# Kernel tuning notes

Measured on AMD Instinct MI355X. Metric: run time of the kernel, lower is better.

The kernel has to match this reference:

```python
import jax, jax.numpy as jnp
import numpy as np

NL, D, DI, N, R, K = 4, 256, 512, 16, 16, 4  # layers, d_model, d_inner, d_state, dt_rank, conv kernel


def setup_inputs() -> dict:
    key = jax.random.key(0)
    ks = jax.random.split(key, 10)
    b, nc, nt = 8, 256, 64
    xc = jax.random.normal(ks[0], (b, nc, D), jnp.float32)
    xt = jax.random.normal(ks[1], (b, nt, D), jnp.float32)
    ln_g = jnp.ones((NL, D), jnp.float32)
    ln_b = jnp.zeros((NL, D), jnp.float32)
    W_in = jax.random.normal(ks[2], (NL, D, 2 * DI), jnp.float32) * (D ** -0.5)
    W_conv = jax.random.normal(ks[3], (NL, DI, 1, K), jnp.float32) * 0.2
    b_conv = jnp.zeros((NL, DI), jnp.float32)
    W_x = jax.random.normal(ks[4], (NL, DI, R + 2 * N), jnp.float32) * (DI ** -0.5)
    W_dt = jax.random.normal(ks[5], (NL, R, DI), jnp.float32) * (R ** -0.5)
    b_dt = jax.random.normal(ks[6], (NL, DI), jnp.float32) * 0.5 - 4.0  # softplus ~ 0.02
    A_log = jnp.broadcast_to(jnp.log(jnp.arange(1, N + 1, dtype=jnp.float32)), (NL, DI, N)).copy()
    Dp = jnp.ones((NL, DI), jnp.float32)
    W_out = jax.random.normal(ks[7], (NL, DI, D), jnp.float32) * (DI ** -0.5)
    return dict(xc=xc, xt=xt, ln_g=ln_g, ln_b=ln_b, W_in=W_in, W_conv=W_conv, b_conv=b_conv,
                W_x=W_x, W_dt=W_dt, b_dt=b_dt, A_log=A_log, Dp=Dp, W_out=W_out)


def _mamba_layer(x, g, beta, Wi, Wc, bc, Wx, Wdt, bdt, Alog, Dvec, Wo):
    # x: [B, L, D]; pre-LN residual Mamba-1 block
    mu = jnp.mean(x, axis=-1, keepdims=True)
    var = jnp.var(x, axis=-1, keepdims=True)
    h = (x - mu) * jax.lax.rsqrt(var + 1e-5) * g + beta
    xz = h @ Wi                              # [B, L, 2*DI]
    xp, z = xz[..., :DI], xz[..., DI:]
    # causal depthwise conv1d
    xcv = jax.lax.conv_general_dilated(xp.transpose(0, 2, 1), Wc, (1,), [(K - 1, 0)],
                                       feature_group_count=DI,
                                       dimension_numbers=('NCH', 'OIH', 'NCH'))
    xcv = jax.nn.silu(xcv.transpose(0, 2, 1) + bc)  # [B, L, DI]
    dbl = xcv @ Wx                           # [B, L, R+2N]
    dt = jax.nn.softplus(dbl[..., :R] @ Wdt + bdt)   # [B, L, DI]
    Bm = dbl[..., R:R + N]                   # [B, L, N]
    Cm = dbl[..., R + N:]                    # [B, L, N]
    A = -jnp.exp(Alog)                       # [DI, N]

    def step(hst, inp):
        x_t, dt_t, b_t, c_t = inp            # [B,DI],[B,DI],[B,N],[B,N]
        dA = jnp.exp(dt_t[:, :, None] * A)   # [B, DI, N]
        hst = dA * hst + (dt_t * x_t)[:, :, None] * b_t[:, None, :]
        return hst, jnp.einsum('bdn,bn->bd', hst, c_t)

    h0 = jnp.zeros((x.shape[0], DI, N), x.dtype)
    _, ys = jax.lax.scan(step, h0, (xcv.transpose(1, 0, 2), dt.transpose(1, 0, 2),
                                    Bm.transpose(1, 0, 2), Cm.transpose(1, 0, 2)))
    y = ys.transpose(1, 0, 2) + xcv * Dvec
    y = y * jax.nn.silu(z)
    return x + y @ Wo


def reference(xc, xt, ln_g, ln_b, W_in, W_conv, b_conv, W_x, W_dt, b_dt, A_log, Dp, W_out):
    b, nc, d = xc.shape
    nt = xt.shape[1]
    # replicate context per target token: [b*nt, nc+1, d]
    xr = jnp.broadcast_to(xc[:, None], (b, nt, nc, d)).reshape(b * nt, nc, d)
    x = jnp.concatenate([xr, xt.reshape(b * nt, 1, d)], axis=1)
    for i in range(NL):
        x = _mamba_layer(x, ln_g[i], ln_b[i], W_in[i], W_conv[i], b_conv[i],
                         W_x[i], W_dt[i], b_dt[i], A_log[i], Dp[i], W_out[i])
    return x[:, -1, :].reshape(b, nt, d)
```

## Files before the change

kernel.cpp:

```cpp
#include <hip/hip_runtime.h>
#include <hip/hip_bf16.h>

#define D_     256
#define TWO_DI 1024
#define DI_    512
#define NSTATE 16
#define RR     16
#define NDBL   48
#define BSEQ   8
#define NC     256
#define NCHUNK 16
#define CLEN   16
#define CTX    2048
#define TGT    512

typedef __attribute__((ext_vector_type(8))) short short8v;
typedef __attribute__((ext_vector_type(8))) unsigned short ushort8v;
typedef __attribute__((ext_vector_type(4))) float floatx4;

__device__ __forceinline__ float siluf(float x) { return x / (1.f + __expf(-x)); }
__device__ __forceinline__ float softplusf(float x) {
  return fmaxf(x, 0.f) + log1pf(__expf(-fabsf(x)));
}
__device__ __forceinline__ unsigned short f2bf(float x) {
// ... 122 lines not shown
  const unsigned short* Bp = &Bt[(size_t)(n0 + srow) * K + schunk];
  ushort8v b0 = *reinterpret_cast<const ushort8v*>(Bp);
  ushort8v b1 = *reinterpret_cast<const ushort8v*>(Bp + 8);
  floatx4 acc[2][2] = {};
#pragma unroll
  for (int j = 0; j < 4; ++j) {
    __syncthreads();
    {
      ushort8v o0, o1;
#pragma unroll
      for (int i = 0; i < 4; ++i) {
        float4 v = xr[j][i];
        unsigned short e0 = f2bf(v.x), e1 = f2bf(v.y), e2 = f2bf(v.z), e3 = f2bf(v.w);
        if (i < 2) { o0[i*4] = (short)e0; o0[i*4+1] = (short)e1; o0[i*4+2] = (short)e2; o0[i*4+3] = (short)e3; }
        else { int jj = (i - 2) * 4; o1[jj] = (short)e0; o1[jj+1] = (short)e1; o1[jj+2] = (short)e2; o1[jj+3] = (short)e3; }
      }
      *reinterpret_cast<ushort8v*>(&As[srow][schunk])     = o0;
      *reinterpret_cast<ushort8v*>(&As[srow][schunk + 8]) = o1;
    }
    *reinterpret_cast<ushort8v*>(&Bs[srow][schunk])     = b0;
    *reinterpret_cast<ushort8v*>(&Bs[srow][schunk + 8]) = b1;
    __syncthreads();
    if (j < 3) {
      b0 = *reinterpret_cast<const ushort8v*>(Bp + j * 64 + 64);
      b1 = *reinterpret_cast<const ushort8v*>(Bp + j * 64 + 72);
    }
#pragma unroll
    for (int ks = 0; ks < 2; ++ks) {
      short8v af2[2], bf2v[2];
#pragma unroll
      for (int f = 0; f < 2; ++f)
        af2[f] = *reinterpret_cast<const short8v*>(&As[wr * 32 + f * 16 + lr][ks * 32 + kq * 8]);
#pragma unroll
      for (int g2 = 0; g2 < 2; ++g2)
        bf2v[g2] = *reinterpret_cast<const short8v*>(&Bs[wc * 32 + g2 * 16 + lr][ks * 32 + kq * 8]);
#pragma unroll
      for (int f = 0; f < 2; ++f)
#pragma unroll
        for (int g2 = 0; g2 < 2; ++g2)
          acc[f][g2] = __builtin_amdgcn_mfma_f32_16x16x32_bf16(af2[f], bf2v[g2], acc[f][g2], 0, 0, 0);
    }
  }
#pragma unroll
  for (int f = 0; f < 2; ++f)
#pragma unroll
    for (int g2 = 0; g2 < 2; ++g2) {
      int col = n0 + wc * 32 + g2 * 16 + lr;
      float c0v = cs0[col], bwv = bW[col];
#pragma unroll
      for (int r = 0; r < 4; ++r) {
        int rowl = wr * 32 + f * 16 + kq * 4 + r;
        int row  = m0 + rowl;
        float v = rstds[rowl] * (acc[f][g2][r] - mus[rowl] * c0v) + bwv;
        if (EPI == 0) {
          C[(size_t)row * N + col] = v;
        } else {
          int bb = row >> 6;
          if (col < DI_) {
            float sv = siluf(cconv[bb * DI_ + col] + v * Wc4[col * 4 + 3]);
            xcv_bf[(size_t)row * DI_ + col] = f2bf(sv);
          } else {
            zbuf[(size_t)row * DI_ + (col - DI_)] = v;
          }
        }
      }
    }
}

template<int EPI>
__global__ __launch_bounds__(256) void gemm_in_ln(
    const float* __restrict__ X, const unsigned short* __restrict__ Bt,
    const float* __restrict__ cs0, const float* __restrict__ bW,
    float* __restrict__ C,
    const float* __restrict__ cconv, const float* __restrict__ Wc4,
    unsigned short* __restrict__ xcv_bf, float* __restrict__ zbuf)
{
  __shared__ unsigned short As[64][72];
  __shared__ unsigned short Bs[64][72];
  __shared__ float mus[64], rstds[64];
  gemm_in_ln_body<EPI>(As, Bs, mus, rstds, blockIdx.x, blockIdx.y,
                       X, Bt, cs0, bW, C, cconv, Wc4, xcv_bf, zbuf);
}

__global__ __launch_bounds__(256) void fused_gemm_in_ln(
    const float* __restrict__ Xa, const unsigned short* __restrict__ Bta,
    const float* __restrict__ cs0a, const float* __restrict__ bWa,
    float* __restrict__ Ca,
    const float* __restrict__ Xb, const unsigned short* __restrict__ Btb,
    const float* __restrict__ cs0b, const float* __restrict__ bWb,
    const float* __restrict__ cconv, const float* __restrict__ Wc4,
    unsigned short* __restrict__ xcv_bf, float* __restrict__ zbuf)
{
  __shared__ unsigned short As[64][72];
  __shared__ unsigned short Bs[64][72];
  __shared__ float mus[64], rstds[64];
  int f = blockIdx.x;
  if (f < 512)
    gemm_in_ln_body<0>(As, Bs, mus, rstds, f & 15, f >> 4, Xa, Bta, cs0a, bWa,
                       Ca, nullptr, nullptr, nullptr, nullptr);
  else {
    f -= 512;
    gemm_in_ln_body<1>(As, Bs, mus, rstds, f & 15, f >> 4, Xb, Btb, cs0b, bWb,
                       nullptr, cconv, Wc4, xcv_bf, zbuf);
  }
}

__global__ __launch_bounds__(256) void gemm_out(
    const unsigned short* __restrict__ A, const unsigned short* __restrict__ Bt,
    const float* __restrict__ resid, float* __restrict__ C, int N, int K)
{
  __shared__ unsigned short As[64][72];
  __shared__ unsigned short Bs[64][72];
  int tid = threadIdx.x;
  int n0 = blockIdx.x * 64, m0 = blockIdx.y * 64;
  int w = tid >> 6, lane = tid & 63;
  int lr = lane & 15, kq = lane >> 4;
  int wr = w >> 1, wc = w & 1;
  int srow = tid >> 2, schunk = (tid & 3) * 16;
  const unsigned short* Ap = &A[(size_t)(m0 + srow) * K + schunk];
  const unsigned short* Bp = &Bt[(size_t)(n0 + srow) * K + schunk];
  ushort8v a0 = *reinterpret_cast<const ushort8v*>(Ap);
  ushort8v a1 = *reinterpret_cast<const ushort8v*>(Ap + 8);
  ushort8v b0 = *reinterpret_cast<const ushort8v*>(Bp);
  ushort8v b1 = *reinterpret_cast<const ushort8v*>(Bp + 8);
  floatx4 acc[2][2] = {};
  for (int k0 = 0; k0 < K; k0 += 64) {
    __syncthreads();
    *reinterpret_cast<ushort8v*>(&As[srow][schunk])     = a0;
    *reinterpret_cast<ushort8v*>(&As[srow][schunk + 8]) = a1;
    *reinterpret_cast<ushort8v*>(&Bs[srow][schunk])     = b0;
    *reinterpret_cast<ushort8v*>(&Bs[srow][schunk + 8]) = b1;
    __syncthreads();
    if (k0 + 64 < K) {
      a0 = *reinterpret_cast<const ushort8v*>(Ap + k0 + 64);
      a1 = *reinterpret_cast<const ushort8v*>(Ap + k0 + 72);
      b0 = *reinterpret_cast<const ushort8v*>(Bp + k0 + 64);
      b1 = *reinterpret_cast<const ushort8v*>(Bp + k0 + 72);
    }
#pragma unroll
    for (int ks = 0; ks < 2; ++ks) {
      short8v af[2], bf2v[2];
#pragma unroll
      for (int f = 0; f < 2; ++f)
        af[f] = *reinterpret_cast<const short8v*>(&As[wr * 32 + f * 16 + lr][ks * 32 + kq * 8]);
#pragma unroll
      for (int g2 = 0; g2 < 2; ++g2)
        bf2v[g2] = *reinterpret_cast<const short8v*>(&Bs[wc * 32 + g2 * 16 + lr][ks * 32 + kq * 8]);
#pragma unroll
      for (int f = 0; f < 2; ++f)
#pragma unroll
        for (int g2 = 0; g2 < 2; ++g2)
          acc[f][g2] = __builtin_amdgcn_mfma_f32_16x16x32_bf16(af[f], bf2v[g2], acc[f][g2], 0, 0, 0);
    }
  }
#pragma unroll
  for (int f = 0; f < 2; ++f)
#pragma unroll
    for (int g2 = 0; g2 < 2; ++g2) {
      int col = n0 + wc * 32 + g2 * 16 + lr;
#pragma unroll
      for (int r = 0; r < 4; ++r) {
        int row = m0 + wr * 32 + f * 16 + kq * 4 + r;
        float v = acc[f][g2][r] + resid[(size_t)row * N + col];
        C[(size_t)row * N + col] = v;
      }
    }
}

__device__ __forceinline__ void gemm_s_body(int bx, int by,
    const unsigned short* __restrict__ A, const unsigned short* __restrict__ Bt,
    const float* __restrict__ resid, float* __restrict__ C, int N, int K)
{
  __shared__ unsigned short As[32][72];
  __shared__ unsigned short Bs[32][72];
  int tid = threadIdx.x;
  int n0 = bx * 32, m0 = by * 32;
  int w = tid >> 6, lane = tid & 63;
  int lr = lane & 15, kq = lane >> 4;
  int wr = w >> 1, wc = w & 1;
  int srow = tid >> 3, schunk = (tid & 7) * 8;
  const unsigned short* Ap = &A[(size_t)(m0 + srow) * K + schunk];
  const unsigned short* Bp = &Bt[(size_t)(n0 + srow) * K + schunk];
  ushort8v a0 = *reinterpret_cast<const ushort8v*>(Ap);
  ushort8v b0 = *reinterpret_cast<const ushort8v*>(Bp);
  floatx4 acc = {};
  for (int k0 = 0; k0 < K; k0 += 64) {
    __syncthreads();
    *reinterpret_cast<ushort8v*>(&As[srow][schunk]) = a0;
    *reinterpret_cast<ushort8v*>(&Bs[srow][schunk]) = b0;
    __syncthreads();
    if (k0 + 64 < K) {
      a0 = *reinterpret_cast<const ushort8v*>(Ap + k0 + 64);
      b0 = *reinterpret_cast<const ushort8v*>(Bp + k0 + 64);
    }
#pragma unroll
    for (int ks = 0; ks < 2; ++ks) {
      short8v af = *reinterpret_cast<const short8v*>(&As[wr * 16 + lr][ks * 32 + kq * 8]);
      short8v bf = *reinterpret_cast<const short8v*>(&Bs[wc * 16 + lr][ks * 32 + kq * 8]);
      acc = __builtin_amdgcn_mfma_f32_16x16x32_bf16(af, bf, acc, 0, 0, 0);
    }
  }
  int col = n0 + wc * 16 + lr;
#pragma unroll
  for (int r = 0; r < 4; ++r) {
    int row = m0 + wr * 16 + kq * 4 + r;
    float v = acc[r] + resid[(size_t)row * N + col];
    C[(size_t)row * N + col] = v;
  }
}

__global__ __launch_bounds__(256) void gemm_s(
    const unsigned short* __restrict__ A, const unsigned short* __restrict__ Bt,
    const float* __restrict__ resid, float* __restrict__ C, int N, int K)
{
  gemm_s_body(blockIdx.x, blockIdx.y, A, Bt, resid, C, N, K);
}

__device__ __forceinline__ void conv_sp_body(int blk,
    const float* __restrict__ xz, const float* __restrict__ Wc,
    const float* __restrict__ bc, const unsigned short* __restrict__ Wxt,
    const float* __restrict__ WdtT, const float* __restrict__ bdt,
    const float* __restrict__ Aneg,
    unsigned short* __restrict__ xcvb, float* __restrict__ dtb,
    float* __restrict__ dblg, float* __restrict__ cconv,
    float* __restrict__ Sb, float* __restrict__ Pb)
{
  __shared__ unsigned short xcs[16][528];
  __shared__ float dbl_s[16][48];
  int seq = blk >> 4, ch = blk & 15;
  int tok0 = blk * 16;
  int tid = threadIdx.x;
  int base = ch * 16;
  float xv_t[2][16], dt_t[2][16];
#pragma unroll
  for (int hh = 0; hh < 2; ++hh) {
    int c = tid + hh * 256;
    const float4 wv = *reinterpret_cast<const float4*>(&Wc[c * 4]);
    float bcv = bc[c];
    const float* xzs = &xz[(size_t)(seq * NC) * TWO_DI + c];
    float r[19];
#pragma unroll
    for (int i = 0; i < 19; ++i) {
      int tl = base - 3 + i;
      r[i] = (tl >= 0) ? xzs[(size_t)tl * TWO_DI] : 0.f;
    }
#pragma unroll
    for (int t = 0; t < 16; ++t) {
      float a = bcv + r[t] * wv.x + r[t + 1] * wv.y + r[t + 2] * wv.z + r[t + 3] * wv.w;
      unsigned short sv = f2bf(siluf(a));
      xcs[t][c] = sv;
      xcvb[(size_t)(tok0 + t) * DI_ + c] = sv;
      xv_t[hh][t] = bf2f(sv);
    }
    if (ch == 15)
      cconv[seq * DI_ + c] = bcv + r[16] * wv.x + r[17] * wv.y + r[18] * wv.z;
  }
  __syncthreads();
  int w = tid >> 6, lane = tid & 63, lr = lane & 15, kq = lane >> 4;
  if (w < 3) {
    floatx4 acc = {};
#pragma unroll
    for (int kc = 0; kc < 16; ++kc) {
      short8v bb = *reinterpret_cast<const short8v*>(&Wxt[(size_t)(w * 16 + lr) * DI_ + kc * 32 + kq * 8]);
      short8v aa = *reinterpret_cast<const short8v*>(&xcs[lr][kc * 32 + kq * 8]);
      acc = __builtin_amdgcn_mfma_f32_16x16x32_bf16(aa, bb, acc, 0, 0, 0);
    }
#pragma unroll
    for (int r2 = 0; r2 < 4; ++r2) {
      int t = kq * 4 + r2, col = w * 16 + lr;
      dbl_s[t][col] = acc[r2];
      dblg[(size_t)(tok0 + t) * NDBL + col] = acc[r2];
    }
  }
  __syncthreads();
#pragma unroll
  for (int hh = 0; hh < 2; ++hh) {
    int c = tid + hh * 256;
    float wr_[16];
    const float4* wt4 = reinterpret_cast<const float4*>(&WdtT[c * 16]);
#pragma unroll
    for (int qq = 0; qq < 4; ++qq) {
      float4 v4 = wt4[qq];
      wr_[qq * 4] = v4.x; wr_[qq * 4 + 1] = v4.y; wr_[qq * 4 + 2] = v4.z; wr_[qq * 4 + 3] = v4.w;
    }
    float bv = bdt[c];
#pragma unroll
    for (int t = 0; t < 16; ++t) {
      float accd = bv;
#pragma unroll
      for (int r2 = 0; r2 < 16; ++r2) accd += dbl_s[t][r2] * wr_[r2];
      float dtv = softplusf(accd);
      dt_t[hh][t] = dtv;
      dtb[(size_t)(tok0 + t) * DI_ + c] = dtv;
    }
  }
#pragma unroll
  for (int hh = 0; hh < 2; ++hh) {
    int d = tid + hh * 256;
    float An[16];
    const float4* An4 = reinterpret_cast<const float4*>(&Aneg[d * NSTATE]);
#pragma unroll
    for (int qq = 0; qq < 4; ++qq) {
      float4 a = An4[qq];
      An[qq * 4] = a.x; An[qq * 4 + 1] = a.y; An[qq * 4 + 2] = a.z; An[qq * 4 + 3] = a.w;
    }
    float h_n[16], p_n[16];
#pragma unroll
    for (int n = 0; n < 16; ++n) { h_n[n] = 0.f; p_n[n] = 1.f; }
#pragma unroll
    for (int t = 0; t < 16; ++t) {
      float dtv  = dt_t[hh][t];
      float coef = dtv * xv_t[hh][t];
      float4 B0 = *reinterpret_cast<const float4*>(&dbl_s[t][RR]);
      float4 B1 = *reinterpret_cast<const float4*>(&dbl_s[t][RR + 4]);
      float4 B2 = *reinterpret_cast<const float4*>(&dbl_s[t][RR + 8]);
      float4 B3 = *reinterpret_cast<const float4*>(&dbl_s[t][RR + 12]);
      float Bv[16] = {B0.x, B0.y, B0.z, B0.w, B1.x, B1.y, B1.z, B1.w,
                      B2.x, B2.y, B2.z, B2.w, B3.x, B3.y, B3.z, B3.w};
#pragma unroll
      for (int n = 0; n < 16; ++n) {
        float dA = __expf(dtv * An[n]);
        h_n[n] = fmaf(dA, h_n[n], coef * Bv[n]);
        p_n[n] *= dA;
      }
    }
    size_t ob = ((size_t)blk * DI_ + d) * NSTATE;
#pragma unroll
    for (int qq = 0; qq < 4; ++qq) {
      *reinterpret_cast<float4*>(&Sb[ob + qq * 4]) =
          make_float4(h_n[qq*4], h_n[qq*4+1], h_n[qq*4+2], h_n[qq*4+3]);
      *reinterpret_cast<float4*>(&Pb[ob + qq * 4]) =
          make_float4(p_n[qq*4], p_n[qq*4+1], p_n[qq*4+2], p_n[qq*4+3]);
    }
  }
}

__global__ __launch_bounds__(256) void conv_sp_kern(
    const float* __restrict__ xz, const float* __restrict__ Wc,
    const float* __restrict__ bc, const unsigned short* __restrict__ Wxt,
    const float* __restrict__ WdtT, const float* __restrict__ bdt,
    const float* __restrict__ Aneg,
    unsigned short* __restrict__ xcvb, float* __restrict__ dtb,
    float* __restrict__ dblg, float* __restrict__ cconv,
    float* __restrict__ Sb, float* __restrict__ Pb)
{
  conv_sp_body(blockIdx.x, xz, Wc, bc, Wxt, WdtT, bdt, Aneg,
               xcvb, dtb, dblg, cconv, Sb, Pb);
}

__device__ __forceinline__ void sf_body(int b,
    const float* __restrict__ dblg, const unsigned short* __restrict__ xcvb,
    const float* __restrict__ xz, const float* __restrict__ dtb,
    const float* __restrict__ Sb, const float* __restrict__ Pb,
    const float* __restrict__ Aneg, const float* __restrict__ Dp,
    unsigned short* __restrict__ yb, float* __restrict__ hstate)
{
  int dg = b & 31, sc = b >> 5;
  int seq = sc >> 4, chunk = sc & 15;
  int tid = threadIdx.x;
  int tt = tid >> 4, cc = tid & 15;
  int tok0 = sc * CLEN;
  __shared__ float dts[16][17], xs[16][17], zs[16][17], Bsh[16][17], Csh[16][17], ys[16][17];
  dts[tt][cc] = dtb[(size_t)(tok0 + tt) * DI_ + dg * 16 + cc];
  xs[tt][cc]  = bf2f(xcvb[(size_t)(tok0 + tt) * DI_ + dg * 16 + cc]);
  zs[tt][cc]  = xz[(size_t)(tok0 + tt) * TWO_DI + DI_ + dg * 16 + cc];
  Bsh[tt][cc] = dblg[(size_t)(tok0 + tt) * NDBL + RR + cc];
  Csh[tt][cc] = dblg[(size_t)(tok0 + tt) * NDBL + RR + NSTATE + cc];
  __syncthreads();
  int dl = tt, n = cc;
  int d = dg * 16 + dl;
  float A  = Aneg[d * NSTATE + n];
  float Dv = Dp[d];
  float Bn[16], Cn[16];
#pragma unroll
  for (int t = 0; t < CLEN; ++t) { Bn[t] = Bsh[t][n]; Cn[t] = Csh[t][n]; }
  float h = 0.f;
  for (int c2 = 0; c2 < chunk; ++c2) {
    size_t o = ((size_t)(seq * NCHUNK + c2) * DI_ + d) * NSTATE + n;
    h = fmaf(Pb[o], h, Sb[o]);
  }
#pragma unroll
  for (int t = 0; t < CLEN; ++t) {
    float dtv = dts[t][dl];
    float xv  = xs[t][dl];
    float dA  = __expf(dtv * A);
    h = fmaf(dA, h, dtv * xv * Bn[t]);
    float p = h * Cn[t];
    p += __shfl_xor(p, 1); p += __shfl_xor(p, 2);
    p += __shfl_xor(p, 4); p += __shfl_xor(p, 8);
    if (n == 0) ys[t][dl] = (p + xv * Dv) * siluf(zs[t][dl]);
  }
  __syncthreads();
  yb[(size_t)(tok0 + tt) * DI_ + dg * 16 + cc] = f2bf(ys[tt][cc]);
  if (chunk == NCHUNK - 1)
    hstate[(size_t)seq * DI_ * NSTATE + d * NSTATE + n] = h;
}

__global__ __launch_bounds__(256) void scan_fin(
    const float* __restrict__ dblg, const unsigned short* __restrict__ xcvb,
    const float* __restrict__ xz, const float* __restrict__ dtb,
    const float* __restrict__ Sb, const float* __restrict__ Pb,
    const float* __restrict__ Aneg, const float* __restrict__ Dp,
    unsigned short* __restrict__ yb, float* __restrict__ hstate)
{
  sf_body(blockIdx.x, dblg, xcvb, xz, dtb, Sb, Pb, Aneg, Dp, yb, hstate);
}

__global__ __launch_bounds__(256) void fused_fin_gout(
    const unsigned short* __restrict__ Ag, const unsigned short* __restrict__ Btg,
    const float* __restrict__ residg, float* __restrict__ Cg,
    const float* __restrict__ dblg, const unsigned short* __restrict__ xcvb,
    const float* __restrict__ xz, const float* __restrict__ dtb,
    const float* __restrict__ Sb, const float* __restrict__ Pb,
    const float* __restrict__ Aneg, const float* __restrict__ Dp,
    unsigned short* __restrict__ yb, float* __restrict__ hstate)
{
  if (blockIdx.x < 128) {
    int f = blockIdx.x;
    gemm_s_body(f & 7, f >> 3, Ag, Btg, residg, Cg, D_, DI_);
  } else {
    sf_body(blockIdx.x - 128, dblg, xcvb, xz, dtb, Sb, Pb, Aneg, Dp, yb, hstate);
  }
}

__device__ __forceinline__ void ssm_body(int blk,
    const unsigned short* __restrict__ xcv_bf, const float* __restrict__ zbuf,
    const unsigned short* __restrict__ Wx, const float* __restrict__ WdtT_l,
    const float* __restrict__ bdt_l, const float* __restrict__ An_l,
    const float* __restrict__ Dp_l, const float* __restrict__ hs,
    unsigned short* __restrict__ ybf)
{
  __shared__ float dbl_s[16][48];
  int tg = blk >> 3, cg = blk & 7;
  int tok0 = tg * 16;
  int b = tg >> 2;
  int tid = threadIdx.x;
  int w = tid >> 6, lane = tid & 63, lr = lane & 15, kq = lane >> 4;
  if (w < 3) {
    floatx4 acc = {};
#pragma unroll
    for (int kc = 0; kc < 16; ++kc) {
      short8v bb = *reinterpret_cast<const short8v*>(&Wx[(size_t)(w * 16 + lr) * DI_ + kc * 32 + kq * 8]);
      short8v aa = *reinterpret_cast<const short8v*>(&xcv_bf[(size_t)(tok0 + lr) * DI_ + kc * 32 + kq * 8]);
      acc = __builtin_amdgcn_mfma_f32_16x16x32_bf16(aa, bb, acc, 0, 0, 0);
    }
#pragma unroll
    for (int r = 0; r < 4; ++r)
      dbl_s[kq * 4 + r][w * 16 + lr] = acc[r];
  }
  __syncthreads();
  int c = cg * 64 + (tid & 63);
  int t0 = (tid >> 6) * 4;
  float wdt_r[16], An[16], hr[16];
  const float4* wt4 = reinterpret_cast<const float4*>(&WdtT_l[c * 16]);
  const float4* An4 = reinterpret_cast<const float4*>(&An_l[c * NSTATE]);
  const float4* hr4 = reinterpret_cast<const float4*>(&hs[(size_t)b * DI_ * NSTATE + c * NSTATE]);
#pragma unroll
  for (int qq = 0; qq < 4; ++qq) {
    float4 wv = wt4[qq]; wdt_r[qq*4]=wv.x; wdt_r[qq*4+1]=wv.y; wdt_r[qq*4+2]=wv.z; wdt_r[qq*4+3]=wv.w;
    float4 a = An4[qq]; An[qq*4]=a.x; An[qq*4+1]=a.y; An[qq*4+2]=a.z; An[qq*4+3]=a.w;
    float4 hv = hr4[qq]; hr[qq*4]=hv.x; hr[qq*4+1]=hv.y; hr[qq*4+2]=hv.z; hr[qq*4+3]=hv.w;
  }
  float Dv = Dp_l[c], bv = bdt_l[c];
#pragma unroll
  for (int tt = 0; tt < 4; ++tt) {
    int t = t0 + tt;
    float accd = bv;
#pragma unroll
    for (int r = 0; r < 16; ++r) accd += dbl_s[t][r] * wdt_r[r];
    float dtv = softplusf(accd);
    float xv = bf2f(xcv_bf[(size_t)(tok0 + t) * DI_ + c]);
    float coef = dtv * xv;
    float y = 0.f;
#pragma unroll
    for (int n = 0; n < 16; ++n) {
      float hn = fmaf(__expf(dtv * An[n]), hr[n], coef * dbl_s[t][RR + n]);
      y = fmaf(hn, dbl_s[t][RR + NSTATE + n], y);
    }
    float yv = (y + xv * Dv) * siluf(zbuf[(size_t)(tok0 + t) * DI_ + c]);
    ybf[(size_t)(tok0 + t) * DI_ + c] = f2bf(yv);
  }
}

__global__ __launch_bounds__(256) void tgt_ssm2(
    const unsigned short* __restrict__ xcv_bf, const float* __restrict__ zbuf,
    const unsigned short* __restrict__ Wx, const float* __restrict__ WdtT_l,
    const float* __restrict__ bdt_l, const float* __restrict__ An_l,
    const float* __restrict__ Dp_l, const float* __restrict__ hs,
    unsigned short* __restrict__ ybf)
{
  ssm_body(blockIdx.x, xcv_bf, zbuf, Wx, WdtT_l, bdt_l, An_l, Dp_l, hs, ybf);
}

__global__ __launch_bounds__(256) void fused_convsp_ssm(
    const float* __restrict__ xz, const float* __restrict__ Wc,
    const float* __restrict__ bc, const unsigned short* __restrict__ WxtA,
    const float* __restrict__ WdtTA, const float* __restrict__ bdtA,
    const float* __restrict__ AnegA,
    unsigned short* __restrict__ xcvb, float* __restrict__ dtb,
    float* __restrict__ dblg, float* __restrict__ cconv,
    float* __restrict__ Sb, float* __restrict__ Pb,
    const unsigned short* __restrict__ xcv_bfB, const float* __restrict__ zbufB,
    const unsigned short* __restrict__ WxB, const float* __restrict__ WdtTB,
    const float* __restrict__ bdtB, const float* __restrict__ AnB,
    const float* __restrict__ DpB, const float* __restrict__ hsB,
    unsigned short* __restrict__ ybfB)
{
  if (blockIdx.x < BSEQ * NCHUNK)
    conv_sp_body(blockIdx.x, xz, Wc, bc, WxtA, WdtTA, bdtA, AnegA,
                 xcvb, dtb, dblg, cconv, Sb, Pb);
  else
    ssm_body(blockIdx.x - BSEQ * NCHUNK, xcv_bfB, zbufB, WxB, WdtTB, bdtB,
             AnB, DpB, hsB, ybfB);
}

extern "C" void kernel_launch(void* const* d_in, const int* in_sizes, int n_in,
                              void* d_out, int out_size, void* d_ws, size_t ws_size,
                              hipStream_t stream)
{
  const float* xc   = (const float*)d_in[0];
  const float* xt   = (const float*)d_in[1];
  const float* ln_g = (const float*)d_in[2];
  const float* ln_b = (const float*)d_in[3];
  const float* W_in = (const float*)d_in[4];
  const float* W_cv = (const float*)d_in[5];
  const float* b_cv = (const float*)d_in[6];
  const float* W_x  = (const float*)d_in[7];
  const float* W_dt = (const float*)d_in[8];
  const float* b_dt = (const float*)d_in[9];
  const float* Alog = (const float*)d_in[10];
  const float* Dp   = (const float*)d_in[11];
  const float* W_o  = (const float*)d_in[12];
  float* out = (float*)d_out;

  float* ws = (float*)d_ws;
  size_t off = 0;
  auto alloc = [&](size_t n) { float* p = ws + off; off += n; return p; };
  float* xz     = alloc((size_t)CTX * TWO_DI);
  float* dtb    = alloc((size_t)CTX * DI_);
  float* dblg   = alloc((size_t)CTX * NDBL);
  float* xcur   = alloc((size_t)CTX * D_);
  float* Sb     = alloc((size_t)BSEQ * NCHUNK * DI_ * NSTATE);
  float* Pb     = alloc((size_t)BSEQ * NCHUNK * DI_ * NSTATE);
  float* cconvT = alloc((size_t)4 * BSEQ * DI_);
  float* hst    = alloc((size_t)4 * BSEQ * DI_ * NSTATE);
  float* Aneg   = alloc((size_t)4 * DI_ * NSTATE);
  float* WdtT   = alloc((size_t)4 * DI_ * RR);
  float* cs0b   = alloc((size_t)4 * TWO_DI);
  float* bWb    = alloc((size_t)4 * TWO_DI);
  float* zbufB  = alloc((size_t)TGT * DI_);
  float* xtb    = alloc((size_t)TGT * D_);
  unsigned short* xcvb    = (unsigned short*)alloc((size_t)CTX * DI_ / 2);
  unsigned short* yb_bf   = (unsigned short*)alloc((size_t)CTX * DI_ / 2);
  unsigned short* xcv_bfB = (unsigned short*)alloc((size_t)TGT * DI_ / 2);
  unsigned short* y_bfB   = (unsigned short*)alloc((size_t)TGT * DI_ / 2);
  unsigned short* Wint    = (unsigned short*)alloc((size_t)4 * TWO_DI * D_ / 2);
  unsigned short* Wot     = (unsigned short*)alloc((size_t)4 * D_ * DI_ / 2);
  unsigned short* Wxt     = (unsigned short*)alloc((size_t)4 * NDBL * DI_ / 2);
  if (off * sizeof(float) > ws_size) return;

  hipMemsetAsync(cs0b, 0, (size_t)8 * TWO_DI * sizeof(float), stream);
  prep_all<<<1920, 256, 0, stream>>>(W_in, W_o, W_x, Alog, W_dt, ln_g, ln_b,
                                     Wint, Wot, Wxt, Aneg, WdtT, cs0b, bWb);

  gemm_in_ln<0><<<dim3(16, CTX / 64), 256, 0, stream>>>(
      xc, Wint, cs0b, bWb, xz, nullptr, nullptr, nullptr, nullptr);
  conv_sp_kern<<<BSEQ * NCHUNK, 256, 0, stream>>>(
      xz, W_cv, b_cv, Wxt, WdtT, b_dt, Aneg, xcvb, dtb, dblg, cconvT, Sb, Pb);
  scan_fin<<<BSEQ * NCHUNK * 32, 256, 0, stream>>>(
      dblg, xcvb, xz, dtb, Sb, Pb, Aneg, Dp, yb_bf, hst);
  gemm_out<<<dim3(D_ / 64, CTX / 64), 256, 0, stream>>>(
      yb_bf, Wot, xc, xcur, D_, DI_);

  for (int l = 0; l < 3; ++l) {
    int la = l + 1;
    const float* xinB = (l == 0) ? xt : xtb;
    fused_gemm_in_ln<<<512 + 128, 256, 0, stream>>>(
        xcur, Wint + (size_t)la * TWO_DI * D_, cs0b + la * TWO_DI, bWb + la * TWO_DI, xz,
        xinB, Wint + (size_t)l * TWO_DI * D_, cs0b + l * TWO_DI, bWb + l * TWO_DI,
        cconvT + (size_t)l * BSEQ * DI_, W_cv + l * DI_ * 4, xcv_bfB, zbufB);
    fused_convsp_ssm<<<BSEQ * NCHUNK + 256, 256, 0, stream>>>(
        xz, W_cv + la * DI_ * 4, b_cv + la * DI_, Wxt + (size_t)la * NDBL * DI_,
        WdtT + (size_t)la * DI_ * RR, b_dt + la * DI_, Aneg + la * DI_ * NSTATE,
        xcvb, dtb, dblg, cconvT + (size_t)la * BSEQ * DI_, Sb, Pb,
        xcv_bfB, zbufB, Wxt + (size_t)l * NDBL * DI_, WdtT + (size_t)l * DI_ * RR,
        b_dt + l * DI_, Aneg + l * DI_ * NSTATE, Dp + l * DI_,
        hst + (size_t)l * BSEQ * DI_ * NSTATE, y_bfB);
    fused_fin_gout<<<128 + BSEQ * NCHUNK * 32, 256, 0, stream>>>(
        y_bfB, Wot + (size_t)l * D_ * DI_, xinB, xtb,
        dblg, xcvb, xz, dtb, Sb, Pb, Aneg + la * DI_ * NSTATE, Dp + la * DI_,
        yb_bf, hst + (size_t)la * BSEQ * DI_ * NSTATE);
    if (la < 3)
      gemm_out<<<dim3(D_ / 64, CTX / 64), 256, 0, stream>>>(
          yb_bf, Wot + (size_t)la * D_ * DI_, xcur, xcur, D_, DI_);
  }

  gemm_in_ln<1><<<dim3(16, TGT / 64), 256, 0, stream>>>(
      xtb, Wint + (size_t)3 * TWO_DI * D_, cs0b + 3 * TWO_DI, bWb + 3 * TWO_DI, nullptr,
      cconvT + (size_t)3 * BSEQ * DI_, W_cv + 3 * DI_ * 4, xcv_bfB, zbufB);
  tgt_ssm2<<<256, 256, 0, stream>>>(xcv_bfB, zbufB,
      Wxt + (size_t)3 * NDBL * DI_, WdtT + (size_t)3 * DI_ * RR, b_dt + 3 * DI_,
      Aneg + 3 * DI_ * NSTATE, Dp + 3 * DI_,
      hst + (size_t)3 * BSEQ * DI_ * NSTATE, y_bfB);
  gemm_s<<<dim3(D_ / 32, TGT / 32), 256, 0, stream>>>(
      y_bfB, Wot + (size_t)3 * D_ * DI_, xtb, out, D_, DI_);
}
```

Measured before the change: 337.0 us.

## Split chunk-local state scan out of conv kernel into a widely parallel kernel

Moves the per-chunk partial scan (chunk-end state S and decay product P) out of the conv kernel. There it ran serially per channel over 16 states in only 128 blocks. It now runs in a separate kernel with 4096 blocks, one thread per (channel, state), which reads dt, xcv and B back from global memory. The intent is to spread the exp-heavy scan across more of the GPU instead of a few register-heavy blocks. In exchange it adds a kernel launch per layer, plus global round-trips of dt, xcv and B, and the scan_fin work is no longer fused with the output GEMM.

```diff
diff --git a/kernel.cpp b/kernel.cpp
--- a/kernel.cpp
+++ b/kernel.cpp
@@ -362,14 +362,12 @@
   gemm_s_body(blockIdx.x, blockIdx.y, A, Bt, resid, C, N, K);
 }
 
-__device__ __forceinline__ void conv_sp_body(int blk,
+__device__ __forceinline__ void conv_body_lean(int blk,
     const float* __restrict__ xz, const float* __restrict__ Wc,
     const float* __restrict__ bc, const unsigned short* __restrict__ Wxt,
     const float* __restrict__ WdtT, const float* __restrict__ bdt,
-    const float* __restrict__ Aneg,
     unsigned short* __restrict__ xcvb, float* __restrict__ dtb,
-    float* __restrict__ dblg, float* __restrict__ cconv,
-    float* __restrict__ Sb, float* __restrict__ Pb)
+    float* __restrict__ dblg, float* __restrict__ cconv)
 {
   __shared__ unsigned short xcs[16][528];
   __shared__ float dbl_s[16][48];
@@ -377,7 +375,6 @@
   int tok0 = blk * 16;
   int tid = threadIdx.x;
   int base = ch * 16;
-  float xv_t[2][16], dt_t[2][16];
 #pragma unroll
   for (int hh = 0; hh < 2; ++hh) {
     int c = tid + hh * 256;
@@ -392,11 +389,10 @@
     }
 #pragma unroll
     for (int t = 0; t < 16; ++t) {
-      float a = bcv + r[t] * wv.x + r[t + 1] * wv.y + r[t + 2] * wv.z + r[t + 3] * wv.w;
-      unsigned short sv = f2bf(siluf(a));
+      float acc = bcv + r[t] * wv.x + r[t + 1] * wv.y + r[t + 2] * wv.z + r[t + 3] * wv.w;
+      unsigned short sv = f2bf(siluf(acc));
       xcs[t][c] = sv;
       xcvb[(size_t)(tok0 + t) * DI_ + c] = sv;
-      xv_t[hh][t] = bf2f(sv);
     }
     if (ch == 15)
       cconv[seq * DI_ + c] = bcv + r[16] * wv.x + r[17] * wv.y + r[18] * wv.z;
@@ -425,9 +421,9 @@
     float wr_[16];
     const float4* wt4 = reinterpret_cast<const float4*>(&WdtT[c * 16]);
 #pragma unroll
-    for (int qq = 0; qq < 4; ++qq) {
-      float4 v4 = wt4[qq];
-      wr_[qq * 4] = v4.x; wr_[qq * 4 + 1] = v4.y; wr_[qq * 4 + 2] = v4.z; wr_[qq * 4 + 3] = v4.w;
+    for (int q = 0; q < 4; ++q) {
+      float4 v4 = wt4[q];
+      wr_[q * 4] = v4.x; wr_[q * 4 + 1] = v4.y; wr_[q * 4 + 2] = v4.z; wr_[q * 4 + 3] = v4.w;
     }
     float bv = bdt[c];
 #pragma unroll
@@ -435,72 +431,84 @@
       float accd = bv;
 #pragma unroll
       for (int r2 = 0; r2 < 16; ++r2) accd += dbl_s[t][r2] * wr_[r2];
-      float dtv = softplusf(accd);
-      dt_t[hh][t] = dtv;
-      dtb[(size_t)(tok0 + t) * DI_ + c] = dtv;
-    }
-  }
-#pragma unroll
-  for (int hh = 0; hh < 2; ++hh) {
-    int d = tid + hh * 256;
-    float An[16];
-    const float4* An4 = reinterpret_cast<const float4*>(&Aneg[d * NSTATE]);
-#pragma unroll
-    for (int qq = 0; qq < 4; ++qq) {
-      float4 a = An4[qq];
-      An[qq * 4] = a.x; An[qq * 4 + 1] = a.y; An[qq * 4 + 2] = a.z; An[qq * 4 + 3] = a.w;
-    }
-    float h_n[16], p_n[16];
-#pragma unroll
-    for (int n = 0; n < 16; ++n) { h_n[n] = 0.f; p_n[n] = 1.f; }
-#pragma unroll
-    for (int t = 0; t < 16; ++t) {
-      float dtv  = dt_t[hh][t];
-      float coef = dtv * xv_t[hh][t];
-      float4 B0 = *reinterpret_cast<const float4*>(&dbl_s[t][RR]);
-      float4 B1 = *reinterpret_cast<const float4*>(&dbl_s[t][RR + 4]);
-      float4 B2 = *reinterpret_cast<const float4*>(&dbl_s[t][RR + 8]);
-      float4 B3 = *reinterpret_cast<const float4*>(&dbl_s[t][RR + 12]);
-      float Bv[16] = {B0.x, B0.y, B0.z, B0.w, B1.x, B1.y, B1.z, B1.w,
-                      B2.x, B2.y, B2.z, B2.w, B3.x, B3.y, B3.z, B3.w};
-#pragma unroll
-      for (int n = 0; n < 16; ++n) {
-        float dA = __expf(dtv * An[n]);
-        h_n[n] = fmaf(dA, h_n[n], coef * Bv[n]);
-        p_n[n] *= dA;
-      }
-    }
-    size_t ob = ((size_t)blk * DI_ + d) * NSTATE;
-#pragma unroll
-    for (int qq = 0; qq < 4; ++qq) {
-      *reinterpret_cast<float4*>(&Sb[ob + qq * 4]) =
-          make_float4(h_n[qq*4], h_n[qq*4+1], h_n[qq*4+2], h_n[qq*4+3]);
-      *reinterpret_cast<float4*>(&Pb[ob + qq * 4]) =
-          make_float4(p_n[qq*4], p_n[qq*4+1], p_n[qq*4+2], p_n[qq*4+3]);
-    }
-  }
-}
-
-__global__ __launch_bounds__(256) void conv_sp_kern(
+      dtb[(size_t)(tok0 + t) * DI_ + c] = softplusf(accd);
+    }
+  }
+}
+
+__global__ __launch_bounds__(256) void conv_lean_kern(
     const float* __restrict__ xz, const float* __restrict__ Wc,
     const float* __restrict__ bc, const unsigned short* __restrict__ Wxt,
     const float* __restrict__ WdtT, const float* __restrict__ bdt,
-    const float* __restrict__ Aneg,
     unsigned short* __restrict__ xcvb, float* __restrict__ dtb,
-    float* __restrict__ dblg, float* __restrict__ cconv,
+    float* __restrict__ dblg, float* __restrict__ cconv)
+{
+  conv_body_lean(blockIdx.x, xz, Wc, bc, Wxt, WdtT, bdt, xcvb, dtb, dblg, cconv);
+}
+
+__device__ __forceinline__ void sp_body(int b,
+    const float* __restrict__ dblg, const unsigned short* __restrict__ xcvb,
+    const float* __restrict__ dtb, const float* __restrict__ Aneg,
     float* __restrict__ Sb, float* __restrict__ Pb)
 {
-  conv_sp_body(blockIdx.x, xz, Wc, bc, Wxt, WdtT, bdt, Aneg,
-               xcvb, dtb, dblg, cconv, Sb, Pb);
-}
-
-__device__ __forceinline__ void sf_body(int b,
+  int dg = b & 31, sc = b >> 5;
+  int tid = threadIdx.x;
+  int tt = tid >> 4, cc = tid & 15;
+  int tok0 = sc * CLEN;
+  __shared__ float dts[16][17], xs[16][17], Bsh[16][17];
+  dts[tt][cc] = dtb[(size_t)(tok0 + tt) * DI_ + dg * 16 + cc];
+  xs[tt][cc]  = bf2f(xcvb[(size_t)(tok0 + tt) * DI_ + dg * 16 + cc]);
+  Bsh[tt][cc] = dblg[(size_t)(tok0 + tt) * NDBL + RR + cc];
+  __syncthreads();
+  int dl = tt, n = cc;
+  int d = dg * 16 + dl;
+  float A = Aneg[d * NSTATE + n];
+  float Bn[16];
+#pragma unroll
+  for (int t = 0; t < CLEN; ++t) Bn[t] = Bsh[t][n];
+  float h = 0.f, p = 1.f;
+#pragma unroll
+  for (int t = 0; t < CLEN; ++t) {
+    float dtv = dts[t][dl];
+    float dA  = __expf(dtv * A);
+    h = fmaf(dA, h, dtv * xs[t][dl] * Bn[t]);
+    p *= dA;
+  }
+  size_t o = ((size_t)sc * DI_ + d) * NSTATE + n;
+  Sb[o] = h; Pb[o] = p;
+}
+
+__global__ __launch_bounds__(256) void sp_kern(
+    const float* __restrict__ dblg, const unsigned short* __restrict__ xcvb,
+    const float* __restrict__ dtb, const float* __restrict__ Aneg,
+    float* __restrict__ Sb, float* __restrict__ Pb)
+{
+  sp_body(blockIdx.x, dblg, xcvb, dtb, Aneg, Sb, Pb);
+}
+
+__global__ __launch_bounds__(256) void fused_sp_gout(
+    const unsigned short* __restrict__ Ag, const unsigned short* __restrict__ Btg,
+    const float* __restrict__ residg, float* __restrict__ Cg,
+    const float* __restrict__ dblg, const unsigned short* __restrict__ xcvb,
+    const float* __restrict__ dtb, const float* __restrict__ Aneg,
+    float* __restrict__ Sb, float* __restrict__ Pb)
+{
+  if (blockIdx.x < 128) {
+    int f = blockIdx.x;
+    gemm_s_body(f & 7, f >> 3, Ag, Btg, residg, Cg, D_, DI_);
+  } else {
+    sp_body(blockIdx.x - 128, dblg, xcvb, dtb, Aneg, Sb, Pb);
+  }
+}
+
+__global__ __launch_bounds__(256) void scan_fin(
     const float* __restrict__ dblg, const unsigned short* __restrict__ xcvb,
     const float* __restrict__ xz, const float* __restrict__ dtb,
     const float* __restrict__ Sb, const float* __restrict__ Pb,
     const float* __restrict__ Aneg, const float* __restrict__ Dp,
     unsigned short* __restrict__ yb, float* __restrict__ hstate)
 {
+  int b = blockIdx.x;
   int dg = b & 31, sc = b >> 5;
   int seq = sc >> 4, chunk = sc & 15;
   int tid = threadIdx.x;
@@ -542,33 +550,6 @@
     hstate[(size_t)seq * DI_ * NSTATE + d * NSTATE + n] = h;
 }
 
-__global__ __launch_bounds__(256) void scan_fin(
-    const float* __restrict__ dblg, const unsigned short* __restrict__ xcvb,
-    const float* __restrict__ xz, const float* __restrict__ dtb,
-    const float* __restrict__ Sb, const float* __restrict__ Pb,
-    const float* __restrict__ Aneg, const float* __restrict__ Dp,
-    unsigned short* __restrict__ yb, float* __restrict__ hstate)
-{
-  sf_body(blockIdx.x, dblg, xcvb, xz, dtb, Sb, Pb, Aneg, Dp, yb, hstate);
-}
-
-__global__ __launch_bounds__(256) void fused_fin_gout(
-    const unsigned short* __restrict__ Ag, const unsigned short* __restrict__ Btg,
-    const float* __restrict__ residg, float* __restrict__ Cg,
-    const float* __restrict__ dblg, const unsigned short* __restrict__ xcvb,
-    const float* __restrict__ xz, const float* __restrict__ dtb,
-    const float* __restrict__ Sb, const float* __restrict__ Pb,
-    const float* __restrict__ Aneg, const float* __restrict__ Dp,
-    unsigned short* __restrict__ yb, float* __restrict__ hstate)
-{
-  if (blockIdx.x < 128) {
-    int f = blockIdx.x;
-    gemm_s_body(f & 7, f >> 3, Ag, Btg, residg, Cg, D_, DI_);
-  } else {
-    sf_body(blockIdx.x - 128, dblg, xcvb, xz, dtb, Sb, Pb, Aneg, Dp, yb, hstate);
-  }
-}
-
 __device__ __forceinline__ void ssm_body(int blk,
     const unsigned short* __restrict__ xcv_bf, const float* __restrict__ zbuf,
     const unsigned short* __restrict__ Wx, const float* __restrict__ WdtT_l,
@@ -638,14 +619,12 @@
   ssm_body(blockIdx.x, xcv_bf, zbuf, Wx, WdtT_l, bdt_l, An_l, Dp_l, hs, ybf);
 }
 
-__global__ __launch_bounds__(256) void fused_convsp_ssm(
+__global__ __launch_bounds__(256) void fused_conv_ssm(
     const float* __restrict__ xz, const float* __restrict__ Wc,
     const float* __restrict__ bc, const unsigned short* __restrict__ WxtA,
     const float* __restrict__ WdtTA, const float* __restrict__ bdtA,
-    const float* __restrict__ AnegA,
     unsigned short* __restrict__ xcvb, float* __restrict__ dtb,
     float* __restrict__ dblg, float* __restrict__ cconv,
-    float* __restrict__ Sb, float* __restrict__ Pb,
     const unsigned short* __restrict__ xcv_bfB, const float* __restrict__ zbufB,
     const unsigned short* __restrict__ WxB, const float* __restrict__ WdtTB,
     const float* __restrict__ bdtB, const float* __restrict__ AnB,
@@ -653,8 +632,8 @@
     unsigned short* __restrict__ ybfB)
 {
   if (blockIdx.x < BSEQ * NCHUNK)
-    conv_sp_body(blockIdx.x, xz, Wc, bc, WxtA, WdtTA, bdtA, AnegA,
-                 xcvb, dtb, dblg, cconv, Sb, Pb);
+    conv_body_lean(blockIdx.x, xz, Wc, bc, WxtA, WdtTA, bdtA,
+                   xcvb, dtb, dblg, cconv);
   else
     ssm_body(blockIdx.x - BSEQ * NCHUNK, xcv_bfB, zbufB, WxB, WdtTB, bdtB,
              AnB, DpB, hsB, ybfB);
@@ -711,8 +690,9 @@
 
   gemm_in_ln<0><<<dim3(16, CTX / 64), 256, 0, stream>>>(
       xc, Wint, cs0b, bWb, xz, nullptr, nullptr, nullptr, nullptr);
-  conv_sp_kern<<<BSEQ * NCHUNK, 256, 0, stream>>>(
-      xz, W_cv, b_cv, Wxt, WdtT, b_dt, Aneg, xcvb, dtb, dblg, cconvT, Sb, Pb);
+  conv_lean_kern<<<BSEQ * NCHUNK, 256, 0, stream>>>(
+      xz, W_cv, b_cv, Wxt, WdtT, b_dt, xcvb, dtb, dblg, cconvT);
+  sp_kern<<<BSEQ * NCHUNK * 32, 256, 0, stream>>>(dblg, xcvb, dtb, Aneg, Sb, Pb);
   scan_fin<<<BSEQ * NCHUNK * 32, 256, 0, stream>>>(
       dblg, xcvb, xz, dtb, Sb, Pb, Aneg, Dp, yb_bf, hst);
   gemm_out<<<dim3(D_ / 64, CTX / 64), 256, 0, stream>>>(
@@ -725,15 +705,17 @@
         xcur, Wint + (size_t)la * TWO_DI * D_, cs0b + la * TWO_DI, bWb + la * TWO_DI, xz,
         xinB, Wint + (size_t)l * TWO_DI * D_, cs0b + l * TWO_DI, bWb + l * TWO_DI,
         cconvT + (size_t)l * BSEQ * DI_, W_cv + l * DI_ * 4, xcv_bfB, zbufB);
-    fused_convsp_ssm<<<BSEQ * NCHUNK + 256, 256, 0, stream>>>(
+    fused_conv_ssm<<<BSEQ * NCHUNK + 256, 256, 0, stream>>>(
         xz, W_cv + la * DI_ * 4, b_cv + la * DI_, Wxt + (size_t)la * NDBL * DI_,
-        WdtT + (size_t)la * DI_ * RR, b_dt + la * DI_, Aneg + la * DI_ * NSTATE,
-        xcvb, dtb, dblg, cconvT + (size_t)la * BSEQ * DI_, Sb, Pb,
+        WdtT + (size_t)la * DI_ * RR, b_dt + la * DI_,
+        xcvb, dtb, dblg, cconvT + (size_t)la * BSEQ * DI_,
         xcv_bfB, zbufB, Wxt + (size_t)l * NDBL * DI_, WdtT + (size_t)l * DI_ * RR,
         b_dt + l * DI_, Aneg + l * DI_ * NSTATE, Dp + l * DI_,
         hst + (size_t)l * BSEQ * DI_ * NSTATE, y_bfB);
-    fused_fin_gout<<<128 + BSEQ * NCHUNK * 32, 256, 0, stream>>>(
+    fused_sp_gout<<<128 + BSEQ * NCHUNK * 32, 256, 0, stream>>>(
         y_bfB, Wot + (size_t)l * D_ * DI_, xinB, xtb,
+        dblg, xcvb, dtb, Aneg + la * DI_ * NSTATE, Sb, Pb);
+    scan_fin<<<BSEQ * NCHUNK * 32, 256, 0, stream>>>(
         dblg, xcvb, xz, dtb, Sb, Pb, Aneg + la * DI_ * NSTATE, Dp + la * DI_,
         yb_bf, hst + (size_t)la * BSEQ * DI_ * NSTATE);
     if (la < 3)
```

After: 304.6 us, median of 3. -9.6%, faster.

## Pair context out-projection with target in-projection and stage conv dt in LDS

Applied to the files above, without the earlier changes.

The cross-layer launch schedule is regrouped. The context out-projection GEMM now shares one launch with the target-branch in-projection/LN/conv (`fused_out_in`), and the context in-projection runs as its own launch. This changes which work overlaps within a launch and removes the trailing standalone target in-projection, but it also runs one extra context out-projection after the last layer whose result is never used. Separately, the conv/x-proj/chunk-scan body keeps dt and the conv outputs in shared memory instead of per-thread register arrays, with the chunk loop no longer unrolled. That is meant to cut register pressure, at the cost of extra LDS traffic and a larger shared-memory footprint.

```diff
diff --git a/kernel.cpp b/kernel.cpp
--- a/kernel.cpp
+++ b/kernel.cpp
@@ -228,37 +228,14 @@
                        X, Bt, cs0, bW, C, cconv, Wc4, xcv_bf, zbuf);
 }
 
-__global__ __launch_bounds__(256) void fused_gemm_in_ln(
-    const float* __restrict__ Xa, const unsigned short* __restrict__ Bta,
-    const float* __restrict__ cs0a, const float* __restrict__ bWa,
-    float* __restrict__ Ca,
-    const float* __restrict__ Xb, const unsigned short* __restrict__ Btb,
-    const float* __restrict__ cs0b, const float* __restrict__ bWb,
-    const float* __restrict__ cconv, const float* __restrict__ Wc4,
-    unsigned short* __restrict__ xcv_bf, float* __restrict__ zbuf)
-{
-  __shared__ unsigned short As[64][72];
-  __shared__ unsigned short Bs[64][72];
-  __shared__ float mus[64], rstds[64];
-  int f = blockIdx.x;
-  if (f < 512)
-    gemm_in_ln_body<0>(As, Bs, mus, rstds, f & 15, f >> 4, Xa, Bta, cs0a, bWa,
-                       Ca, nullptr, nullptr, nullptr, nullptr);
-  else {
-    f -= 512;
-    gemm_in_ln_body<1>(As, Bs, mus, rstds, f & 15, f >> 4, Xb, Btb, cs0b, bWb,
-                       nullptr, cconv, Wc4, xcv_bf, zbuf);
-  }
-}
-
-__global__ __launch_bounds__(256) void gemm_out(
+__device__ __forceinline__ void gemm_out_body(int bx, int by,
     const unsigned short* __restrict__ A, const unsigned short* __restrict__ Bt,
     const float* __restrict__ resid, float* __restrict__ C, int N, int K)
 {
   __shared__ unsigned short As[64][72];
   __shared__ unsigned short Bs[64][72];
   int tid = threadIdx.x;
-  int n0 = blockIdx.x * 64, m0 = blockIdx.y * 64;
+  int n0 = bx * 64, m0 = by * 64;
   int w = tid >> 6, lane = tid & 63;
   int lr = lane & 15, kq = lane >> 4;
   int wr = w >> 1, wc = w & 1;
@@ -313,6 +290,27 @@
     }
 }
 
+__global__ __launch_bounds__(256) void fused_out_in(
+    const unsigned short* __restrict__ Ag, const unsigned short* __restrict__ Btg,
+    const float* __restrict__ residg, float* __restrict__ Cg,
+    const float* __restrict__ Xb, const unsigned short* __restrict__ Btb,
+    const float* __restrict__ cs0, const float* __restrict__ bW,
+    const float* __restrict__ cconv, const float* __restrict__ Wc4,
+    unsigned short* __restrict__ xcv_bf, float* __restrict__ zbuf)
+{
+  int f = blockIdx.x;
+  if (f < 128) {
+    gemm_out_body(f & 3, f >> 2, Ag, Btg, residg, Cg, D_, DI_);
+  } else {
+    __shared__ unsigned short As[64][72];
+    __shared__ unsigned short Bs[64][72];
+    __shared__ float mus[64], rstds[64];
+    f -= 128;
+    gemm_in_ln_body<1>(As, Bs, mus, rstds, f & 15, f >> 4, Xb, Btb, cs0, bW,
+                       nullptr, cconv, Wc4, xcv_bf, zbuf);
+  }
+}
+
 __device__ __forceinline__ void gemm_s_body(int bx, int by,
     const unsigned short* __restrict__ A, const unsigned short* __restrict__ Bt,
     const float* __restrict__ resid, float* __restrict__ C, int N, int K)
@@ -362,7 +360,7 @@
   gemm_s_body(blockIdx.x, blockIdx.y, A, Bt, resid, C, N, K);
 }
 
-__device__ __forceinline__ void conv_sp_body(int blk,
+__device__ __forceinline__ void conv_sp2_body(int blk,
     const float* __restrict__ xz, const float* __restrict__ Wc,
     const float* __restrict__ bc, const unsigned short* __restrict__ Wxt,
     const float* __restrict__ WdtT, const float* __restrict__ bdt,
@@ -372,12 +370,12 @@
     float* __restrict__ Sb, float* __restrict__ Pb)
 {
   __shared__ unsigned short xcs[16][528];
+  __shared__ float dts_s[16][520];
   __shared__ float dbl_s[16][48];
   int seq = blk >> 4, ch = blk & 15;
   int tok0 = blk * 16;
   int tid = threadIdx.x;
   int base = ch * 16;
-  float xv_t[2][16], dt_t[2][16];
 #pragma unroll
   for (int hh = 0; hh < 2; ++hh) {
     int c = tid + hh * 256;
@@ -396,26 +394,27 @@
       unsigned short sv = f2bf(siluf(a));
       xcs[t][c] = sv;
       xcvb[(size_t)(tok0 + t) * DI_ + c] = sv;
-      xv_t[hh][t] = bf2f(sv);
     }
     if (ch == 15)
       cconv[seq * DI_ + c] = bcv + r[16] * wv.x + r[17] * wv.y + r[18] * wv.z;
   }
   __syncthreads();
-  int w = tid >> 6, lane = tid & 63, lr = lane & 15, kq = lane >> 4;
-  if (w < 3) {
-    floatx4 acc = {};
-#pragma unroll
-    for (int kc = 0; kc < 16; ++kc) {
-      short8v bb = *reinterpret_cast<const short8v*>(&Wxt[(size_t)(w * 16 + lr) * DI_ + kc * 32 + kq * 8]);
-      short8v aa = *reinterpret_cast<const short8v*>(&xcs[lr][kc * 32 + kq * 8]);
-      acc = __builtin_amdgcn_mfma_f32_16x16x32_bf16(aa, bb, acc, 0, 0, 0);
-    }
-#pragma unroll
-    for (int r2 = 0; r2 < 4; ++r2) {
-      int t = kq * 4 + r2, col = w * 16 + lr;
-      dbl_s[t][col] = acc[r2];
-      dblg[(size_t)(tok0 + t) * NDBL + col] = acc[r2];
+  {
+    int w = tid >> 6, lane = tid & 63, lr = lane & 15, kq = lane >> 4;
+    if (w < 3) {
+      floatx4 acc = {};
+#pragma unroll
+      for (int kc = 0; kc < 16; ++kc) {
+        short8v bb = *reinterpret_cast<const short8v*>(&Wxt[(size_t)(w * 16 + lr) * DI_ + kc * 32 + kq * 8]);
+        short8v aa = *reinterpret_cast<const short8v*>(&xcs[lr][kc * 32 + kq * 8]);
+        acc = __builtin_amdgcn_mfma_f32_16x16x32_bf16(aa, bb, acc, 0, 0, 0);
+      }
+#pragma unroll
+      for (int r2 = 0; r2 < 4; ++r2) {
+        int t = kq * 4 + r2, col = w * 16 + lr;
+        dbl_s[t][col] = acc[r2];
+        dblg[(size_t)(tok0 + t) * NDBL + col] = acc[r2];
+      }
     }
   }
   __syncthreads();
@@ -436,11 +435,12 @@
 #pragma unroll
       for (int r2 = 0; r2 < 16; ++r2) accd += dbl_s[t][r2] * wr_[r2];
       float dtv = softplusf(accd);
-      dt_t[hh][t] = dtv;
+      dts_s[t][c] = dtv;
       dtb[(size_t)(tok0 + t) * DI_ + c] = dtv;
     }
   }
-#pragma unroll
+  __syncthreads();
+#pragma unroll 1
   for (int hh = 0; hh < 2; ++hh) {
     int d = tid + hh * 256;
     float An[16];
@@ -453,16 +453,15 @@
     float h_n[16], p_n[16];
 #pragma unroll
     for (int n = 0; n < 16; ++n) { h_n[n] = 0.f; p_n[n] = 1.f; }
-#pragma unroll
     for (int t = 0; t < 16; ++t) {
-      float dtv  = dt_t[hh][t];
-      float coef = dtv * xv_t[hh][t];
-      float4 B0 = *reinterpret_cast<const float4*>(&dbl_s[t][RR]);
-      float4 B1 = *reinterpret_cast<const float4*>(&dbl_s[t][RR + 4]);
-      float4 B2 = *reinterpret_cast<const float4*>(&dbl_s[t][RR + 8]);
-      float4 B3 = *reinterpret_cast<const float4*>(&dbl_s[t][RR + 12]);
-      float Bv[16] = {B0.x, B0.y, B0.z, B0.w, B1.x, B1.y, B1.z, B1.w,
-                      B2.x, B2.y, B2.z, B2.w, B3.x, B3.y, B3.z, B3.w};
+      float dtv  = dts_s[t][d];
+      float coef = dtv * bf2f(xcs[t][d]);
+      float Bv[16];
+#pragma unroll
+      for (int qq = 0; qq < 4; ++qq) {
+        float4 b4 = *reinterpret_cast<const float4*>(&dbl_s[t][RR + qq * 4]);
+        Bv[qq * 4] = b4.x; Bv[qq * 4 + 1] = b4.y; Bv[qq * 4 + 2] = b4.z; Bv[qq * 4 + 3] = b4.w;
+      }
 #pragma unroll
       for (int n = 0; n < 16; ++n) {
         float dA = __expf(dtv * An[n]);
@@ -481,7 +480,7 @@
   }
 }
 
-__global__ __launch_bounds__(256) void conv_sp_kern(
+__global__ __launch_bounds__(256) void conv_sp2_kern(
     const float* __restrict__ xz, const float* __restrict__ Wc,
     const float* __restrict__ bc, const unsigned short* __restrict__ Wxt,
     const float* __restrict__ WdtT, const float* __restrict__ bdt,
@@ -490,8 +489,8 @@
     float* __restrict__ dblg, float* __restrict__ cconv,
     float* __restrict__ Sb, float* __restrict__ Pb)
 {
-  conv_sp_body(blockIdx.x, xz, Wc, bc, Wxt, WdtT, bdt, Aneg,
-               xcvb, dtb, dblg, cconv, Sb, Pb);
+  conv_sp2_body(blockIdx.x, xz, Wc, bc, Wxt, WdtT, bdt, Aneg,
+                xcvb, dtb, dblg, cconv, Sb, Pb);
 }
 
 __device__ __forceinline__ void sf_body(int b,
@@ -653,8 +652,8 @@
     unsigned short* __restrict__ ybfB)
 {
   if (blockIdx.x < BSEQ * NCHUNK)
-    conv_sp_body(blockIdx.x, xz, Wc, bc, WxtA, WdtTA, bdtA, AnegA,
-                 xcvb, dtb, dblg, cconv, Sb, Pb);
+    conv_sp2_body(blockIdx.x, xz, Wc, bc, WxtA, WdtTA, bdtA, AnegA,
+                  xcvb, dtb, dblg, cconv, Sb, Pb);
   else
     ssm_body(blockIdx.x - BSEQ * NCHUNK, xcv_bfB, zbufB, WxB, WdtTB, bdtB,
              AnB, DpB, hsB, ybfB);
@@ -711,39 +710,37 @@
 
   gemm_in_ln<0><<<dim3(16, CTX / 64), 256, 0, stream>>>(
       xc, Wint, cs0b, bWb, xz, nullptr, nullptr, nullptr, nullptr);
-  conv_sp_kern<<<BSEQ * NCHUNK, 256, 0, stream>>>(
+  conv_sp2_kern<<<BSEQ * NCHUNK, 256, 0, stream>>>(
       xz, W_cv, b_cv, Wxt, WdtT, b_dt, Aneg, xcvb, dtb, dblg, cconvT, Sb, Pb);
   scan_fin<<<BSEQ * NCHUNK * 32, 256, 0, stream>>>(
       dblg, xcvb, xz, dtb, Sb, Pb, Aneg, Dp, yb_bf, hst);
-  gemm_out<<<dim3(D_ / 64, CTX / 64), 256, 0, stream>>>(
-      yb_bf, Wot, xc, xcur, D_, DI_);
-
-  for (int l = 0; l < 3; ++l) {
-    int la = l + 1;
-    const float* xinB = (l == 0) ? xt : xtb;
-    fused_gemm_in_ln<<<512 + 128, 256, 0, stream>>>(
-        xcur, Wint + (size_t)la * TWO_DI * D_, cs0b + la * TWO_DI, bWb + la * TWO_DI, xz,
-        xinB, Wint + (size_t)l * TWO_DI * D_, cs0b + l * TWO_DI, bWb + l * TWO_DI,
+  fused_out_in<<<256, 256, 0, stream>>>(
+      yb_bf, Wot, xc, xcur,
+      xt, Wint, cs0b, bWb, cconvT, W_cv, xcv_bfB, zbufB);
+
+  for (int l = 1; l < 4; ++l) {
+    int lb = l - 1;
+    const float* residB = (lb == 0) ? xt : xtb;
+    gemm_in_ln<0><<<dim3(16, CTX / 64), 256, 0, stream>>>(
+        xcur, Wint + (size_t)l * TWO_DI * D_, cs0b + l * TWO_DI, bWb + l * TWO_DI,
+        xz, nullptr, nullptr, nullptr, nullptr);
+    fused_convsp_ssm<<<BSEQ * NCHUNK + 256, 256, 0, stream>>>(
+        xz, W_cv + l * DI_ * 4, b_cv + l * DI_, Wxt + (size_t)l * NDBL * DI_,
+        WdtT + (size_t)l * DI_ * RR, b_dt + l * DI_, Aneg + l * DI_ * NSTATE,
+        xcvb, dtb, dblg, cconvT + (size_t)l * BSEQ * DI_, Sb, Pb,
+        xcv_bfB, zbufB, Wxt + (size_t)lb * NDBL * DI_, WdtT + (size_t)lb * DI_ * RR,
+        b_dt + lb * DI_, Aneg + lb * DI_ * NSTATE, Dp + lb * DI_,
+        hst + (size_t)lb * BSEQ * DI_ * NSTATE, y_bfB);
+    fused_fin_gout<<<128 + BSEQ * NCHUNK * 32, 256, 0, stream>>>(
+        y_bfB, Wot + (size_t)lb * D_ * DI_, residB, xtb,
+        dblg, xcvb, xz, dtb, Sb, Pb, Aneg + l * DI_ * NSTATE, Dp + l * DI_,
+        yb_bf, hst + (size_t)l * BSEQ * DI_ * NSTATE);
+    fused_out_in<<<256, 256, 0, stream>>>(
+        yb_bf, Wot + (size_t)l * D_ * DI_, xcur, xcur,
+        xtb, Wint + (size_t)l * TWO_DI * D_, cs0b + l * TWO_DI, bWb + l * TWO_DI,
         cconvT + (size_t)l * BSEQ * DI_, W_cv + l * DI_ * 4, xcv_bfB, zbufB);
-    fused_convsp_ssm<<<BSEQ * NCHUNK + 256, 256, 0, stream>>>(
-        xz, W_cv + la * DI_ * 4, b_cv + la * DI_, Wxt + (size_t)la * NDBL * DI_,
-        WdtT + (size_t)la * DI_ * RR, b_dt + la * DI_, Aneg + la * DI_ * NSTATE,
-        xcvb, dtb, dblg, cconvT + (size_t)la * BSEQ * DI_, Sb, Pb,
-        xcv_bfB, zbufB, Wxt + (size_t)l * NDBL * DI_, WdtT + (size_t)l * DI_ * RR,
-        b_dt + l * DI_, Aneg + l * DI_ * NSTATE, Dp + l * DI_,
-        hst + (size_t)l * BSEQ * DI_ * NSTATE, y_bfB);
-    fused_fin_gout<<<128 + BSEQ * NCHUNK * 32, 256, 0, stream>>>(
-        y_bfB, Wot + (size_t)l * D_ * DI_, xinB, xtb,
-        dblg, xcvb, xz, dtb, Sb, Pb, Aneg + la * DI_ * NSTATE, Dp + la * DI_,
-        yb_bf, hst + (size_t)la * BSEQ * DI_ * NSTATE);
-    if (la < 3)
-      gemm_out<<<dim3(D_ / 64, CTX / 64), 256, 0, stream>>>(
-          yb_bf, Wot + (size_t)la * D_ * DI_, xcur, xcur, D_, DI_);
-  }
-
-  gemm_in_ln<1><<<dim3(16, TGT / 64), 256, 0, stream>>>(
-      xtb, Wint + (size_t)3 * TWO_DI * D_, cs0b + 3 * TWO_DI, bWb + 3 * TWO_DI, nullptr,
-      cconvT + (size_t)3 * BSEQ * DI_, W_cv + 3 * DI_ * 4, xcv_bfB, zbufB);
+  }
+
   tgt_ssm2<<<256, 256, 0, stream>>>(xcv_bfB, zbufB,
       Wxt + (size_t)3 * NDBL * DI_, WdtT + (size_t)3 * DI_ * RR, b_dt + 3 * DI_,
       Aneg + 3 * DI_ * NSTATE, Dp + 3 * DI_,
```

Result: faster. 313.7 us (-6.9%).
